# Optimization experiments

Hardware: AMD Instinct MI355X
Metric: run time of the kernel (lower is better)

The kernel has to match this reference:

```python
import jax, jax.numpy as jnp
import numpy as np
from jax import lax

H = 64
IN = 3

def _lstm_layer(x, Wih, Whh, bih, bhh, collect):
    # x: [B, T, in]; Wih: [4H, in]; Whh: [4H, H]. PyTorch gate order: i, f, g, o.
    B = x.shape[0]
    h0 = jnp.zeros((B, H), x.dtype)
    c0 = jnp.zeros((B, H), x.dtype)
    b = bih + bhh
    def step(carry, xt):
        h, c = carry
        gates = xt @ Wih.T + h @ Whh.T + b  # [B, 4H]
        i, f, g, o = jnp.split(gates, 4, axis=-1)
        i = jax.nn.sigmoid(i); f = jax.nn.sigmoid(f)
        g = jnp.tanh(g); o = jax.nn.sigmoid(o)
        c = f * c + i * g
        h = o * jnp.tanh(c)
        return (h, c), (h if collect else None)
    xs = jnp.swapaxes(x, 0, 1)  # [T, B, in]
    (h, c), hs = lax.scan(step, (h0, c0), xs)
    if collect:
        return jnp.swapaxes(hs, 0, 1)  # [B, T, H]
    return h  # [B, H]


def setup_inputs() -> dict:
    key = jax.random.key(0)
    ks = jax.random.split(key, 14)
    s = 1.0 / np.sqrt(H)
    def u(k, shape):
        return jax.random.uniform(k, shape, jnp.float32, -s, s)
    return {
        "x": jax.random.normal(ks[0], (4096, 512, IN), jnp.float32),
        "Wih0": u(ks[1], (4 * H, IN)), "Whh0": u(ks[2], (4 * H, H)),
        "bih0": u(ks[3], (4 * H,)), "bhh0": u(ks[4], (4 * H,)),
        "Wih1": u(ks[5], (4 * H, H)), "Whh1": u(ks[6], (4 * H, H)),
        "bih1": u(ks[7], (4 * H,)), "bhh1": u(ks[8], (4 * H,)),
        "Wc1": jax.random.normal(ks[9], (32, H), jnp.float32) * 0.1,
        "bc1": jnp.zeros((32,), jnp.float32),
        "Wc2": jax.random.normal(ks[10], (1, 32), jnp.float32) * 0.1,
        "bc2": jnp.zeros((1,), jnp.float32),
    }


def reference(x, Wih0, Whh0, bih0, bhh0, Wih1, Whh1, bih1, bhh1, Wc1, bc1, Wc2, bc2):
    # 2-layer LSTM (dropout inactive at inference); only last timestep of layer 2 is used.
    h1 = _lstm_layer(x, Wih0, Whh0, bih0, bhh0, collect=True)   # [B, T, H]
    last = _lstm_layer(h1, Wih1, Whh1, bih1, bhh1, collect=False)  # [B, H]
    hidden = jax.nn.relu(last @ Wc1.T + bc1)  # [B, 32]
    out = jax.nn.sigmoid(hidden @ Wc2.T + bc2)  # [B, 1]
    return out
```

## Files before the change

kernel.cpp:

```cpp
#include <hip/hip_runtime.h>

#define TSEQ   512
#define BATCH  4096
#define MROWS  16

typedef short bf16x8 __attribute__((ext_vector_type(8)));
typedef short bf16x4 __attribute__((ext_vector_type(4)));
typedef float f32x4  __attribute__((ext_vector_type(4)));
typedef float f32x2  __attribute__((ext_vector_type(2)));

#define NL2E  (-1.44269504f)
#define P2L2E (2.88539008f)

__device__ __forceinline__ unsigned short f2bf(float f) {
    unsigned int u = __builtin_bit_cast(unsigned int, f);
    return (unsigned short)((u + 0x8000u) >> 16);
}

__device__ __forceinline__ f32x2 cellupd2(const f32x4 a, const f32x4 b, f32x2& C) {
    f32x2 ei = {__builtin_amdgcn_exp2f(a[0]), __builtin_amdgcn_exp2f(b[0])};
    f32x2 ef = {__builtin_amdgcn_exp2f(a[1]), __builtin_amdgcn_exp2f(b[1])};
    f32x2 eg = {__builtin_amdgcn_exp2f(a[2]), __builtin_amdgcn_exp2f(b[2])};
    f32x2 eo = {__builtin_amdgcn_exp2f(a[3]), __builtin_amdgcn_exp2f(b[3])};
    f32x2 A  = 1.f + ei;
    f32x2 G1 = eg + 1.f;
    f32x2 F  = 1.f + ef;
    f32x2 t  = A * G1;
    f32x2 G2 = eg * P2L2E + (NL2E * 2.f);
    f32x2 num = C * t + G2 * F;
    f32x2 den = t * F;
    f32x2 r  = {__builtin_amdgcn_rcpf(den.x), __builtin_amdgcn_rcpf(den.y)};
    f32x2 Cn = num * r;
    Cn.x = fminf(Cn.x, 126.f);
    Cn.y = fminf(Cn.y, 126.f);
    C = Cn;
    f32x2 ec = {__builtin_amdgcn_exp2f(Cn.x), __builtin_amdgcn_exp2f(Cn.y)};
    f32x2 B  = 1.f + eo;
    f32x2 hn = ec - 1.f;
    f32x2 hd = B * (ec + 1.f);
    f32x2 rr = {__builtin_amdgcn_rcpf(hd.x), __builtin_amdgcn_rcpf(hd.y)};
    return hn * rr;
}


__global__ __launch_bounds__(1024, 4) void lstm2_kernel(
    const float* __restrict__ x,
    const float* __restrict__ Wih0, const float* __restrict__ Whh0,
    const float* __restrict__ bih0, const float* __restrict__ bhh0,
    const float* __restrict__ Wih1, const float* __restrict__ Whh1,
    const float* __restrict__ bih1, const float* __restrict__ bhh1,
    const float* __restrict__ Wc1,  const float* __restrict__ bc1,
    const float* __restrict__ Wc2,  const float* __restrict__ bc2,
    float* __restrict__ out)
{
    __shared__ __align__(16) unsigned short ring[2][MROWS * 64];
    __shared__ __align__(16) unsigned short h2s[2][MROWS * 64];
    __shared__ __align__(16) unsigned short xq[64][128];
    __shared__ float h2f[MROWS][65];
    __shared__ float hid[MROWS][33];

    const int tid  = threadIdx.x;
    const int wv   = tid >> 6;
    const int lane = tid & 63;
    const int col  = lane & 15;
    const int lg   = lane >> 4;
    const int b0   = blockIdx.x * MROWS;
    const int sw   = (col & 7) << 4;

    ((unsigned int*)ring)[tid] = 0u;
    ((unsigned int*)h2s)[tid]  = 0u;

    const int xrow = (tid >> 5) & 15;
    const int xt   = tid & 31;
    const float* xb = x + ((size_t)(b0 + xrow) * TSEQ + xt) * 3;
    float xr0 = 0.f, xr1 = 0.f, xr2 = 0.f;
    if (tid < 512) {
        xr0 = xb[0]; xr1 = xb[1]; xr2 = xb[2];
        bf16x8 xf = {(short)f2bf(xr0),(short)f2bf(xr1),(short)f2bf(xr2),0,0,0,0,0};
        *(bf16x8*)((char*)xq + (xt << 8) + ((xrow << 4) ^ ((xt & 7) << 4))) = xf;
        xr0 = xb[96]; xr1 = xb[97]; xr2 = xb[98];
    }
    __syncthreads();

    const int rd0 = (col * 128 +      lg * 16) ^ sw;
    const int rd1 = (col * 128 + 64 + lg * 16) ^ sw;

#define FLUSH(S) do { \
    if (((S) & 31) == 16 && (S) < 480) { \
        const int c1_ = ((S) >> 5) + 1; \
        const int t64_ = ((c1_ & 1) << 5) + xt; \
        bf16x8 xf_ = {(short)f2bf(xr0),(short)f2bf(xr1),(short)f2bf(xr2),0,0,0,0,0}; \
        *(bf16x8*)((char*)xq + (t64_ << 8) + ((xrow << 4) ^ ((xt & 7) << 4))) = xf_; \
        if (c1_ < 15) { const float* p_ = xb + (c1_ + 1) * 96; xr0 = p_[0]; xr1 = p_[1]; xr2 = p_[2]; } \
    } \
} while(0)

    if (wv < 8) {
        const int wq = wv;
        const int ga = col & 3;
        const float sca = (ga == 2) ? P2L2E : NL2E;
        bf16x8 Wf[2][3];
        f32x4 bia4[2];
#pragma unroll
        for (int tt = 0; tt < 2; ++tt) {
            const int n = ga * 64 + 16 * (col >> 2) + 2 * wq + tt;
#pragma unroll
            for (int f = 0; f < 3; ++f)
#pragma unroll
                for (int i = 0; i < 8; ++i) {
                    const int k = f * 32 + lg * 8 + i;
                    float v = 0.f;
                    if (k < 64)      v = Whh0[n * 64 + k];
                    else if (k < 67) v = Wih0[n * 3 + (k - 64)];
                    Wf[tt][f][i] = (short)f2bf(sca * v);
                }
#pragma unroll
            for (int r = 0; r < 4; ++r) {
                const int nb = r * 64 + 16 * lg + 2 * wq + tt;
                bia4[tt][r] = ((r == 2) ? P2L2E : NL2E) * (bih0[nb] + bhh0[nb]);
            }
        }
        const int hw = (col * 128 + 32 * lg + 4 * wq) ^ sw;
        f32x2 C01 = {0.f, 0.f};

#define L1B(RI, WI, S) do { \
        const char* rb_ = (const char*)ring[RI]; \
        bf16x8 v0_ = *(const bf16x8*)(rb_ + rd0); \
        bf16x8 v1_ = *(const bf16x8*)(rb_ + rd1); \
        bf16x8 v2_ = {0,0,0,0,0,0,0,0}; \
        if (lg == 0) \
            v2_ = *(const bf16x8*)((const char*)xq + ((((S)&63)) << 8) + ((col << 4) ^ (((S)&7) << 4))); \
        f32x4 a0_ = __builtin_amdgcn_mfma_f32_16x16x32_bf16(Wf[0][0], v0_, bia4[0],0,0,0); \
        f32x4 a1_ = __builtin_amdgcn_mfma_f32_16x16x32_bf16(Wf[1][0], v0_, bia4[1],0,0,0); \
        a0_ = __builtin_amdgcn_mfma_f32_16x16x32_bf16(Wf[0][1], v1_, a0_,0,0,0); \
        a1_ = __builtin_amdgcn_mfma_f32_16x16x32_bf16(Wf[1][1], v1_, a1_,0,0,0); \
        a0_ = __builtin_amdgcn_mfma_f32_16x16x32_bf16(Wf[0][2], v2_, a0_,0,0,0); \
        a1_ = __builtin_amdgcn_mfma_f32_16x16x32_bf16(Wf[1][2], v2_, a1_,0,0,0); \
        f32x2 h01_ = cellupd2(a0_, a1_, C01); \
        unsigned int p0_; \
        asm("v_cvt_pk_bf16_f32 %0, %1, %2" : "=v"(p0_) : "v"(h01_.x), "v"(h01_.y)); \
        *(unsigned int*)((char*)ring[WI] + hw) = p0_; \
    } while(0)

        L1B(1, 0, 0);
        __syncthreads();
#pragma unroll 1
        for (int m = 0; m < 255; ++m) {
            const int s1 = 2 * m + 1;
            L1B(0, 1, s1);
            __syncthreads();
            L1B(1, 0, s1 + 1);
            FLUSH(s1 + 1);
            __syncthreads();
        }
        L1B(0, 1, 511);
        __syncthreads();
        __syncthreads();
#undef L1B
    } else {
        const int wq = wv - 8;
        const int ga = col & 3;
        const float sca = (ga == 2) ? P2L2E : NL2E;
        bf16x8 Wf[2][4];
        f32x4 bia4[2];
#pragma unroll
        for (int tt = 0; tt < 2; ++tt) {
            const int n = ga * 64 + 16 * (col >> 2) + 2 * wq + tt;
#pragma unroll
            for (int f = 0; f < 4; ++f)
#pragma unroll
                for (int i = 0; i < 8; ++i) {
                    const int k = f * 32 + lg * 8 + i;
                    const float v = (k < 64) ? Wih1[n * 64 + k] : Whh1[n * 64 + (k - 64)];
                    Wf[tt][f][i] = (short)f2bf(sca * v);
                }
#pragma unroll
            for (int r = 0; r < 4; ++r) {
                const int nb = r * 64 + 16 * lg + 2 * wq + tt;
                bia4[tt][r] = ((r == 2) ? P2L2E : NL2E) * (bih1[nb] + bhh1[nb]);
            }
        }
        const int hw2 = (col * 128 + 32 * lg + 4 * wq) ^ sw;
        f32x2 C01 = {0.f, 0.f};
        f32x2 hv01 = {0.f, 0.f};

#define L2B(RB, HR) do { \
        const char* rb_ = (const char*)ring[RB]; \
        const char* hp_ = (const char*)h2s[HR]; \
        bf16x8 v0_ = *(const bf16x8*)(rb_ + rd0); \
        bf16x8 v1_ = *(const bf16x8*)(rb_ + rd1); \
        bf16x8 v2_ = *(const bf16x8*)(hp_ + rd0); \
        bf16x8 v3_ = *(const bf16x8*)(hp_ + rd1); \
        f32x4 a0_ = __builtin_amdgcn_mfma_f32_16x16x32_bf16(Wf[0][0], v0_, bia4[0],0,0,0); \
        f32x4 a1_ = __builtin_amdgcn_mfma_f32_16x16x32_bf16(Wf[1][0], v0_, bia4[1],0,0,0); \
        a0_ = __builtin_amdgcn_mfma_f32_16x16x32_bf16(Wf[0][1], v1_, a0_,0,0,0); \
        a1_ = __builtin_amdgcn_mfma_f32_16x16x32_bf16(Wf[1][1], v1_, a1_,0,0,0); \
        a0_ = __builtin_amdgcn_mfma_f32_16x16x32_bf16(Wf[0][2], v2_, a0_,0,0,0); \
        a1_ = __builtin_amdgcn_mfma_f32_16x16x32_bf16(Wf[1][2], v2_, a1_,0,0,0); \
        a0_ = __builtin_amdgcn_mfma_f32_16x16x32_bf16(Wf[0][3], v3_, a0_,0,0,0); \
        a1_ = __builtin_amdgcn_mfma_f32_16x16x32_bf16(Wf[1][3], v3_, a1_,0,0,0); \
        hv01 = cellupd2(a0_, a1_, C01); \
        unsigned int p0_; \
        asm("v_cvt_pk_bf16_f32 %0, %1, %2" : "=v"(p0_) : "v"(hv01.x), "v"(hv01.y)); \
        *(unsigned int*)((char*)h2s[RB] + hw2) = p0_; \
    } while(0)

        __syncthreads();
#pragma unroll 1
        for (int m = 0; m < 255; ++m) {
            L2B(0, 1);
            __syncthreads();
            L2B(1, 0);
            __syncthreads();
        }
        L2B(0, 1);
        __syncthreads();
        L2B(1, 0);
        __syncthreads();
#undef L2B
        const int ub = 16 * lg + 2 * wq;
        h2f[col][ub + 0] = hv01.x;
        h2f[col][ub + 1] = hv01.y;
    }
    __syncthreads();

    if (tid < 512) {
        const int b = tid & 15, j = tid >> 4;
        float s = bc1[j];
#pragma unroll 8
        for (int k = 0; k < 64; ++k) s += Wc1[j * 64 + k] * h2f[b][k];
        hid[b][j] = fmaxf(s, 0.f);
    }
    __syncthreads();
    if (tid < 16) {
        float s = bc2[0];
#pragma unroll 8
        for (int k = 0; k < 32; ++k) s += Wc2[k] * hid[tid][k];
        float e = __builtin_amdgcn_exp2f(NL2E * s);
        out[b0 + tid] = __builtin_amdgcn_rcpf(1.f + e);
    }
}

extern "C" void kernel_launch(void* const* d_in, const int* in_sizes, int n_in,
                              void* d_out, int out_size, void* d_ws, size_t ws_size,
                              hipStream_t stream) {
    lstm2_kernel<<<BATCH / MROWS, 1024, 0, stream>>>(
        (const float*)d_in[0],
        (const float*)d_in[1], (const float*)d_in[2],
        (const float*)d_in[3], (const float*)d_in[4],
        (const float*)d_in[5], (const float*)d_in[6],
        (const float*)d_in[7], (const float*)d_in[8],
        (const float*)d_in[9], (const float*)d_in[10],
        (const float*)d_in[11], (const float*)d_in[12],
        (float*)d_out);
}
```

Measured before the change: 293.3 us.

## Prefetch x tile across steps, permute hidden layout, and raise MFMA wave priority

Each timestep now reads the x input fragment one step ahead and issues its MFMA first, so that LDS read is off the recurrence critical path. The lg==0 branch is removed, so all lanes read xq, where before only one lane group did. The hidden-state write offsets are rearranged and the weight columns are permuted to match, presumably to get better-coalesced LDS stores. The compute section is wrapped in s_setprio, and the FLUSH of upcoming x is moved before the second step of each pair. These add LDS traffic and scheduling complexity in exchange for shorter serial step latency.

```diff
diff --git a/kernel.cpp b/kernel.cpp
--- a/kernel.cpp
+++ b/kernel.cpp
@@ -5,7 +5,6 @@
 #define MROWS  16
 
 typedef short bf16x8 __attribute__((ext_vector_type(8)));
-typedef short bf16x4 __attribute__((ext_vector_type(4)));
 typedef float f32x4  __attribute__((ext_vector_type(4)));
 typedef float f32x2  __attribute__((ext_vector_type(2)));
 
@@ -15,6 +14,10 @@
 __device__ __forceinline__ unsigned short f2bf(float f) {
     unsigned int u = __builtin_bit_cast(unsigned int, f);
     return (unsigned short)((u + 0x8000u) >> 16);
+}
+
+__device__ __forceinline__ int uperm(int p) {
+    return 16 * ((p >> 1) & 3) + 2 * (p >> 3) + (p & 1);
 }
 
 __device__ __forceinline__ f32x2 cellupd2(const f32x4 a, const f32x4 b, f32x2& C) {
@@ -95,6 +98,9 @@
     } \
 } while(0)
 
+#define XQRD(S) (*(const bf16x8*)((const char*)xq + ((((S)&63)) << 8) + ((col << 4) ^ (((S)&7) << 4))))
+#define MM(A,B,C) __builtin_amdgcn_mfma_f32_16x16x32_bf16((A),(B),(C),0,0,0)
+
     if (wv < 8) {
         const int wq = wv;
         const int ga = col & 3;
@@ -110,7 +116,7 @@
                 for (int i = 0; i < 8; ++i) {
                     const int k = f * 32 + lg * 8 + i;
                     float v = 0.f;
-                    if (k < 64)      v = Whh0[n * 64 + k];
+                    if (k < 64)      v = Whh0[n * 64 + uperm(k)];
                     else if (k < 67) v = Wih0[n * 3 + (k - 64)];
                     Wf[tt][f][i] = (short)f2bf(sca * v);
                 }
@@ -120,26 +126,27 @@
                 bia4[tt][r] = ((r == 2) ? P2L2E : NL2E) * (bih0[nb] + bhh0[nb]);
             }
         }
-        const int hw = (col * 128 + 32 * lg + 4 * wq) ^ sw;
+        const int hw = (col * 128 + 16 * wq + 4 * lg) ^ sw;
         f32x2 C01 = {0.f, 0.f};
+        bf16x8 pv2 = XQRD(0);
 
 #define L1B(RI, WI, S) do { \
         const char* rb_ = (const char*)ring[RI]; \
         bf16x8 v0_ = *(const bf16x8*)(rb_ + rd0); \
         bf16x8 v1_ = *(const bf16x8*)(rb_ + rd1); \
-        bf16x8 v2_ = {0,0,0,0,0,0,0,0}; \
-        if (lg == 0) \
-            v2_ = *(const bf16x8*)((const char*)xq + ((((S)&63)) << 8) + ((col << 4) ^ (((S)&7) << 4))); \
-        f32x4 a0_ = __builtin_amdgcn_mfma_f32_16x16x32_bf16(Wf[0][0], v0_, bia4[0],0,0,0); \
-        f32x4 a1_ = __builtin_amdgcn_mfma_f32_16x16x32_bf16(Wf[1][0], v0_, bia4[1],0,0,0); \
-        a0_ = __builtin_amdgcn_mfma_f32_16x16x32_bf16(Wf[0][1], v1_, a0_,0,0,0); \
-        a1_ = __builtin_amdgcn_mfma_f32_16x16x32_bf16(Wf[1][1], v1_, a1_,0,0,0); \
-        a0_ = __builtin_amdgcn_mfma_f32_16x16x32_bf16(Wf[0][2], v2_, a0_,0,0,0); \
-        a1_ = __builtin_amdgcn_mfma_f32_16x16x32_bf16(Wf[1][2], v2_, a1_,0,0,0); \
+        __builtin_amdgcn_s_setprio(1); \
+        f32x4 a0_ = MM(Wf[0][2], pv2, bia4[0]); \
+        f32x4 a1_ = MM(Wf[1][2], pv2, bia4[1]); \
+        a0_ = MM(Wf[0][0], v0_, a0_); \
+        a1_ = MM(Wf[1][0], v0_, a1_); \
+        a0_ = MM(Wf[0][1], v1_, a0_); \
+        a1_ = MM(Wf[1][1], v1_, a1_); \
+        pv2 = XQRD((S) + 1); \
         f32x2 h01_ = cellupd2(a0_, a1_, C01); \
         unsigned int p0_; \
         asm("v_cvt_pk_bf16_f32 %0, %1, %2" : "=v"(p0_) : "v"(h01_.x), "v"(h01_.y)); \
         *(unsigned int*)((char*)ring[WI] + hw) = p0_; \
+        __builtin_amdgcn_s_setprio(0); \
     } while(0)
 
         L1B(1, 0, 0);
@@ -149,8 +156,8 @@
             const int s1 = 2 * m + 1;
             L1B(0, 1, s1);
             __syncthreads();
+            FLUSH(s1 + 1);
             L1B(1, 0, s1 + 1);
-            FLUSH(s1 + 1);
             __syncthreads();
         }
         L1B(0, 1, 511);
@@ -171,7 +178,8 @@
 #pragma unroll
                 for (int i = 0; i < 8; ++i) {
                     const int k = f * 32 + lg * 8 + i;
-                    const float v = (k < 64) ? Wih1[n * 64 + k] : Whh1[n * 64 + (k - 64)];
+                    const float v = (k < 64) ? Wih1[n * 64 + uperm(k)]
+                                             : Whh1[n * 64 + uperm(k - 64)];
                     Wf[tt][f][i] = (short)f2bf(sca * v);
                 }
 #pragma unroll
@@ -180,7 +188,7 @@
                 bia4[tt][r] = ((r == 2) ? P2L2E : NL2E) * (bih1[nb] + bhh1[nb]);
             }
         }
-        const int hw2 = (col * 128 + 32 * lg + 4 * wq) ^ sw;
+        const int hw2 = (col * 128 + 16 * wq + 4 * lg) ^ sw;
         f32x2 C01 = {0.f, 0.f};
         f32x2 hv01 = {0.f, 0.f};
 
@@ -191,18 +199,20 @@
         bf16x8 v1_ = *(const bf16x8*)(rb_ + rd1); \
         bf16x8 v2_ = *(const bf16x8*)(hp_ + rd0); \
         bf16x8 v3_ = *(const bf16x8*)(hp_ + rd1); \
-        f32x4 a0_ = __builtin_amdgcn_mfma_f32_16x16x32_bf16(Wf[0][0], v0_, bia4[0],0,0,0); \
-        f32x4 a1_ = __builtin_amdgcn_mfma_f32_16x16x32_bf16(Wf[1][0], v0_, bia4[1],0,0,0); \
-        a0_ = __builtin_amdgcn_mfma_f32_16x16x32_bf16(Wf[0][1], v1_, a0_,0,0,0); \
-        a1_ = __builtin_amdgcn_mfma_f32_16x16x32_bf16(Wf[1][1], v1_, a1_,0,0,0); \
-        a0_ = __builtin_amdgcn_mfma_f32_16x16x32_bf16(Wf[0][2], v2_, a0_,0,0,0); \
-        a1_ = __builtin_amdgcn_mfma_f32_16x16x32_bf16(Wf[1][2], v2_, a1_,0,0,0); \
-        a0_ = __builtin_amdgcn_mfma_f32_16x16x32_bf16(Wf[0][3], v3_, a0_,0,0,0); \
-        a1_ = __builtin_amdgcn_mfma_f32_16x16x32_bf16(Wf[1][3], v3_, a1_,0,0,0); \
+        __builtin_amdgcn_s_setprio(1); \
+        f32x4 a0_ = MM(Wf[0][0], v0_, bia4[0]); \
+        f32x4 a1_ = MM(Wf[1][0], v0_, bia4[1]); \
+        a0_ = MM(Wf[0][1], v1_, a0_); \
+        a1_ = MM(Wf[1][1], v1_, a1_); \
+        a0_ = MM(Wf[0][2], v2_, a0_); \
+        a1_ = MM(Wf[1][2], v2_, a1_); \
+        a0_ = MM(Wf[0][3], v3_, a0_); \
+        a1_ = MM(Wf[1][3], v3_, a1_); \
         hv01 = cellupd2(a0_, a1_, C01); \
         unsigned int p0_; \
         asm("v_cvt_pk_bf16_f32 %0, %1, %2" : "=v"(p0_) : "v"(hv01.x), "v"(hv01.y)); \
         *(unsigned int*)((char*)h2s[RB] + hw2) = p0_; \
+        __builtin_amdgcn_s_setprio(0); \
     } while(0)
 
         __syncthreads();
```

New measurement: 288.6 us (median of 2 runs). Within noise of the previous version (-1.6%).
